# Performance work log

Hardware: AMD Instinct MI355X
Metric: run time of the kernel (lower is better)

## Reference

```python
import jax, jax.numpy as jnp
import numpy as np


def _chamfer(x, y):
    # x: [B, N, 3], y: [B, M, 3]
    x2 = jnp.sum(x * x, axis=-1)                      # [B, N]
    y2 = jnp.sum(y * y, axis=-1)                      # [B, M]
    xy = jnp.einsum('bnd,bmd->bnm', x, y)             # [B, N, M]
    d = x2[:, :, None] + y2[:, None, :] - 2.0 * xy    # [B, N, M]
    cham_x = jnp.min(d, axis=2).mean(axis=1)          # nearest y for each x
    cham_y = jnp.min(d, axis=1).mean(axis=1)          # nearest x for each y
    # pytorch3d default: mean over points, mean over batch, sum of both directions
    return jnp.mean(cham_x + cham_y)


def setup_inputs() -> dict:
    key = jax.random.key(0)
    kx, ky = jax.random.split(key)
    B, N, M, D = 4, 8192, 8192, 3
    x = jax.random.normal(kx, (B, N, D), dtype=jnp.float32)
    y = jax.random.normal(ky, (B, M, D), dtype=jnp.float32)
    return {"x": x, "y": y}


def reference(x, y):
    return _chamfer(x, y)
```

## Files before the change

### kernel.cpp

```cpp
#include <hip/hip_runtime.h>


#define BATCH   4
#define NPTS    8192
#define TPB     256
#define CSLICE  512
#define QT      4
#define QBLK    (4 * QT * 32)
#define MT      (CSLICE / 32)
#define SLICES  (NPTS / CSLICE)
#define QBLKS   (NPTS / QBLK)

typedef _Float16 h8   __attribute__((ext_vector_type(8)));
typedef float    f16v __attribute__((ext_vector_type(16)));

__device__ __forceinline__ void split16(float v, _Float16& hi, _Float16& lo) {
    hi = (_Float16)v;
    lo = (_Float16)(v - (float)hi);
}

__device__ __forceinline__ float tree16(const f16v& d) {
    float g0 = fminf(fminf(d[0],  d[1]),  d[2]);
    float g1 = fminf(fminf(d[3],  d[4]),  d[5]);
    float g2 = fminf(fminf(d[6],  d[7]),  d[8]);
    float g3 = fminf(fminf(d[9],  d[10]), d[11]);
    float g4 = fminf(fminf(d[12], d[13]), d[14]);
    float h0 = fminf(fminf(g0, g1), d[15]);
    float h1 = fminf(fminf(g2, g3), g4);
    return fminf(h0, h1);
}

__global__ __launch_bounds__(TPB, 8) void chamfer_mfma(const float* __restrict__ xg,
                                                       const float* __restrict__ yg,
                                                       float* __restrict__ partial,
                                                       float* __restrict__ out) {
    __shared__ h8 afrag[CSLICE * 2];

    const int tid    = threadIdx.x;
    const int qblock = blockIdx.x;
    const int slice  = blockIdx.y & (SLICES - 1);
    const int b      = blockIdx.y >> 4;
    const int dir    = blockIdx.z;
    const int lane   = tid & 63, wave = tid >> 6;
    const int col    = lane & 31, hv = lane >> 5;

    if (tid == 0) out[0] = 0.0f;
    const float* q = dir ? yg : xg;
    const float* r = dir ? xg : yg;

    const float* rbase = r + ((size_t)b * NPTS + slice * CSLICE) * 3;
#pragma unroll
    for (int i = 0; i < CSLICE / TPB; ++i) {
        const int p = tid + i * TPB;
        float r0 = rbase[p * 3 + 0], r1 = rbase[p * 3 + 1], r2 = rbase[p * 3 + 2];
        _Float16 h0, l0, h1, l1, h2, l2, rnh, rnl;
        split16(r0, h0, l0);
        split16(r1, h1, l1);
        split16(r2, h2, l2);
        split16(fmaf(r0, r0, fmaf(r1, r1, r2 * r2)), rnh, rnl);
        const int base = (p >> 5) * 64 + (p & 31);
        afrag[base]      = (h8){h0, h1, h2, l0, l1, l2, h0, h1};
        afrag[base + 32] = (h8){h2, rnh, rnl, (_Float16)1.0f, (_Float16)1.0f,
                                (_Float16)0.0f, (_Float16)0.0f, (_Float16)0.0f};
    }

    h8 bq[QT];
#pragma unroll
    for (int t = 0; t < QT; ++t) {
        const int qi = qblock * QBLK + (wave * QT + t) * 32 + col;
        const float* qp = q + ((size_t)b * NPTS + qi) * 3;
        float x0 = qp[0], x1 = qp[1], x2 = qp[2];
        _Float16 H0, L0, H1, L1, H2, L2, qnh, qnl;
        split16(-2.0f * x0, H0, L0);
        split16(-2.0f * x1, H1, L1);
        split16(-2.0f * x2, H2, L2);
        split16(fmaf(x0, x0, fmaf(x1, x1, x2 * x2)), qnh, qnl);
        h8 b0 = {H0, H1, H2, H0, H1, H2, L0, L1};
        h8 b1 = {L2, (_Float16)1.0f, (_Float16)1.0f, qnh, qnl,
                 (_Float16)0.0f, (_Float16)0.0f, (_Float16)0.0f};
        bq[t] = hv ? b1 : b0;
    }
    __syncthreads();

    float cm[QT];
#pragma unroll
    for (int t = 0; t < QT; ++t) cm[t] = 3.0e38f;

    for (int mt = 0; mt < MT; ++mt) {
        const h8 ar = afrag[mt * 64 + lane];
        f16v d0, d1;
        asm("v_mfma_f32_32x32x16_f16 %0, %2, %3, 0\n\t"
            "v_mfma_f32_32x32x16_f16 %1, %2, %4, 0\n\t"
            "s_nop 7\n\t"
            "s_nop 7"
            : "=v"(d0), "=v"(d1)
            : "v"(ar), "v"(bq[0]), "v"(bq[1]));
        cm[0] = fminf(cm[0], tree16(d0));
        cm[1] = fminf(cm[1], tree16(d1));

        f16v d2, d3;
        asm("v_mfma_f32_32x32x16_f16 %0, %2, %3, 0\n\t"
            "v_mfma_f32_32x32x16_f16 %1, %2, %4, 0\n\t"
            "s_nop 7\n\t"
            "s_nop 7"
            : "=v"(d2), "=v"(d3)
            : "v"(ar), "v"(bq[2]), "v"(bq[3]));
        cm[2] = fminf(cm[2], tree16(d2));
        cm[3] = fminf(cm[3], tree16(d3));
    }

    float* pp = partial + ((size_t)(dir * BATCH + b) * SLICES + slice) * NPTS
                        + qblock * QBLK;
#pragma unroll
    for (int t = 0; t < QT; ++t) {
        cm[t] = fminf(cm[t], __shfl_xor(cm[t], 32, 64));
        if (hv == 0)
            pp[(wave * QT + t) * 32 + col] = cm[t];
    }
}

__global__ __launch_bounds__(TPB) void chamfer_reduce(const float* __restrict__ partial,
                                                      float* __restrict__ out) {
    const int tid = threadIdx.x;
    const int g   = blockIdx.x * TPB + tid;
    const int db  = g >> 13;
    const int n   = g & (NPTS - 1);

    const float* p = partial + (size_t)db * SLICES * NPTS + n;
    float v = 3.0e38f;
#pragma unroll
    for (int s = 0; s < SLICES; ++s)
        v = fminf(v, p[(size_t)s * NPTS]);

    float w = v;
#pragma unroll
    for (int off = 32; off > 0; off >>= 1)
        w += __shfl_down(w, off, 64);
    __shared__ float ss[TPB / 64];
    if ((tid & 63) == 0) ss[tid >> 6] = w;
    __syncthreads();
    if (tid == 0)
        atomicAdd(out, (ss[0] + ss[1] + ss[2] + ss[3]) * (1.0f / (float)(BATCH * NPTS)));
}

extern "C" void kernel_launch(void* const* d_in, const int* in_sizes, int n_in,
                              void* d_out, int out_size, void* d_ws, size_t ws_size,
                              hipStream_t stream) {
    const float* x = (const float*)d_in[0];
    const float* y = (const float*)d_in[1];
    float* out = (float*)d_out;
    float* partial = (float*)d_ws;

    chamfer_mfma<<<dim3(QBLKS, BATCH * SLICES, 2), TPB, 0, stream>>>(x, y, partial, out);
    chamfer_reduce<<<dim3(2 * BATCH * NPTS / TPB), TPB, 0, stream>>>(partial, out);
}
```

Measured before the change: 77.36 us.

## Precompute fp16 split fragments once and fuse final reduction via last-block counter

Adds a presplit kernel that converts every point of x and y once into the hi/lo fp16 MFMA A and B fragments and stores them in workspace. The main kernel now copies those fragments straight into LDS and registers instead of recomputing the split per block. The separate reduce kernel is removed: each query-block group counts finished slices with an atomic counter, and the last block reduces the partial minima and adds into the output. This trades the redundant conversion and one launch for an extra launch, extra fragment traffic, and atomic/fence overhead.

```diff
diff --git a/kernel.cpp b/kernel.cpp
--- a/kernel.cpp
+++ b/kernel.cpp
@@ -10,6 +10,7 @@
 #define MT      (CSLICE / 32)
 #define SLICES  (NPTS / CSLICE)
 #define QBLKS   (NPTS / QBLK)
+#define FR_PER_SB 16384
 
 typedef _Float16 h8   __attribute__((ext_vector_type(8)));
 typedef float    f16v __attribute__((ext_vector_type(16)));
@@ -30,11 +31,53 @@
     return fminf(h0, h1);
 }
 
-__global__ __launch_bounds__(TPB, 8) void chamfer_mfma(const float* __restrict__ xg,
-                                                       const float* __restrict__ yg,
+__global__ __launch_bounds__(TPB) void chamfer_presplit(const float* __restrict__ xg,
+                                                        const float* __restrict__ yg,
+                                                        h8* __restrict__ aArr,
+                                                        h8* __restrict__ bArr,
+                                                        unsigned* __restrict__ cnt,
+                                                        float* __restrict__ out) {
+    const int tid = threadIdx.x;
+    const int g   = blockIdx.x * TPB + tid;
+    if (blockIdx.x == 0) {
+        if (tid < 2 * BATCH * QBLKS) cnt[tid] = 0u;
+        if (tid == 0) out[0] = 0.0f;
+    }
+    const int b = g >> 13, i = g & (NPTS - 1);
+#pragma unroll
+    for (int s = 0; s < 2; ++s) {
+        const float* p = (s ? yg : xg) + ((size_t)b * NPTS + i) * 3;
+        float c0 = p[0], c1 = p[1], c2 = p[2];
+        _Float16 h0, l0, h1, l1, h2, l2, nh, nl, H0, L0, H1, L1, H2, L2;
+        split16(c0, h0, l0);
+        split16(c1, h1, l1);
+        split16(c2, h2, l2);
+        split16(fmaf(c0, c0, fmaf(c1, c1, c2 * c2)), nh, nl);
+        split16(-2.0f * c0, H0, L0);
+        split16(-2.0f * c1, H1, L1);
+        split16(-2.0f * c2, H2, L2);
+        const size_t base = (size_t)(s * BATCH + b) * FR_PER_SB;
+        aArr[base + (i >> 5) * 64 + (i & 31)]      =
+            (h8){h0, h1, h2, l0, l1, l2, h0, h1};
+        aArr[base + (i >> 5) * 64 + 32 + (i & 31)] =
+            (h8){h2, nh, nl, (_Float16)1.0f, (_Float16)1.0f,
+                 (_Float16)0.0f, (_Float16)0.0f, (_Float16)0.0f};
+        bArr[base + i * 2]     =
+            (h8){H0, H1, H2, H0, H1, H2, L0, L1};
+        bArr[base + i * 2 + 1] =
+            (h8){L2, (_Float16)1.0f, (_Float16)1.0f, nh, nl,
+                 (_Float16)0.0f, (_Float16)0.0f, (_Float16)0.0f};
+    }
+}
+
+__global__ __launch_bounds__(TPB, 8) void chamfer_mfma(const h8* __restrict__ aArr,
+                                                       const h8* __restrict__ bArr,
                                                        float* __restrict__ partial,
+                                                       unsigned* __restrict__ cnt,
                                                        float* __restrict__ out) {
     __shared__ h8 afrag[CSLICE * 2];
+    __shared__ float sred[TPB / 64];
+    __shared__ int sflag;
 
     const int tid    = threadIdx.x;
     const int qblock = blockIdx.x;
@@ -44,41 +87,20 @@
     const int lane   = tid & 63, wave = tid >> 6;
     const int col    = lane & 31, hv = lane >> 5;
 
-    if (tid == 0) out[0] = 0.0f;
-    const float* q = dir ? yg : xg;
-    const float* r = dir ? xg : yg;
+    const int sa = dir ? 0 : 1;
+    const int sb = dir ? 1 : 0;
 
-    const float* rbase = r + ((size_t)b * NPTS + slice * CSLICE) * 3;
+    const h8* asrc = aArr + (size_t)(sa * BATCH + b) * FR_PER_SB + slice * (CSLICE * 2);
 #pragma unroll
-    for (int i = 0; i < CSLICE / TPB; ++i) {
-        const int p = tid + i * TPB;
-        float r0 = rbase[p * 3 + 0], r1 = rbase[p * 3 + 1], r2 = rbase[p * 3 + 2];
-        _Float16 h0, l0, h1, l1, h2, l2, rnh, rnl;
-        split16(r0, h0, l0);
-        split16(r1, h1, l1);
-        split16(r2, h2, l2);
-        split16(fmaf(r0, r0, fmaf(r1, r1, r2 * r2)), rnh, rnl);
-        const int base = (p >> 5) * 64 + (p & 31);
-        afrag[base]      = (h8){h0, h1, h2, l0, l1, l2, h0, h1};
-        afrag[base + 32] = (h8){h2, rnh, rnl, (_Float16)1.0f, (_Float16)1.0f,
-                                (_Float16)0.0f, (_Float16)0.0f, (_Float16)0.0f};
-    }
+    for (int i2 = 0; i2 < (CSLICE * 2) / TPB; ++i2)
+        afrag[tid + i2 * TPB] = asrc[tid + i2 * TPB];
 
+    const h8* bsrc = bArr + (size_t)(sb * BATCH + b) * FR_PER_SB;
     h8 bq[QT];
 #pragma unroll
     for (int t = 0; t < QT; ++t) {
         const int qi = qblock * QBLK + (wave * QT + t) * 32 + col;
-        const float* qp = q + ((size_t)b * NPTS + qi) * 3;
-        float x0 = qp[0], x1 = qp[1], x2 = qp[2];
-        _Float16 H0, L0, H1, L1, H2, L2, qnh, qnl;
-        split16(-2.0f * x0, H0, L0);
-        split16(-2.0f * x1, H1, L1);
-        split16(-2.0f * x2, H2, L2);
-        split16(fmaf(x0, x0, fmaf(x1, x1, x2 * x2)), qnh, qnl);
-        h8 b0 = {H0, H1, H2, H0, H1, H2, L0, L1};
-        h8 b1 = {L2, (_Float16)1.0f, (_Float16)1.0f, qnh, qnl,
-                 (_Float16)0.0f, (_Float16)0.0f, (_Float16)0.0f};
-        bq[t] = hv ? b1 : b0;
+        bq[t] = bsrc[qi * 2 + hv];
     }
     __syncthreads();
 
@@ -109,38 +131,46 @@
         cm[3] = fminf(cm[3], tree16(d3));
     }
 
-    float* pp = partial + ((size_t)(dir * BATCH + b) * SLICES + slice) * NPTS
+    float* pw = partial + ((size_t)(dir * BATCH + b) * SLICES + slice) * NPTS
                         + qblock * QBLK;
 #pragma unroll
     for (int t = 0; t < QT; ++t) {
         cm[t] = fminf(cm[t], __shfl_xor(cm[t], 32, 64));
         if (hv == 0)
-            pp[(wave * QT + t) * 32 + col] = cm[t];
+            pw[(wave * QT + t) * 32 + col] = cm[t];
     }
-}
 
-__global__ __launch_bounds__(TPB) void chamfer_reduce(const float* __restrict__ partial,
-                                                      float* __restrict__ out) {
-    const int tid = threadIdx.x;
-    const int g   = blockIdx.x * TPB + tid;
-    const int db  = g >> 13;
-    const int n   = g & (NPTS - 1);
+    __syncthreads();
+    const int group = (dir * BATCH + b) * QBLKS + qblock;
+    if (tid == 0) {
+        __threadfence();
+        unsigned old = __hip_atomic_fetch_add(&cnt[group], 1u, __ATOMIC_ACQ_REL,
+                                              __HIP_MEMORY_SCOPE_AGENT);
+        sflag = (old == (unsigned)(SLICES - 1)) ? 1 : 0;
+    }
+    __syncthreads();
+    if (!sflag) return;
 
-    const float* p = partial + (size_t)db * SLICES * NPTS + n;
-    float v = 3.0e38f;
+    const float* pr = partial + (size_t)(dir * BATCH + b) * SLICES * NPTS
+                              + qblock * QBLK;
+    float sum = 0.0f;
 #pragma unroll
-    for (int s = 0; s < SLICES; ++s)
-        v = fminf(v, p[(size_t)s * NPTS]);
-
-    float w = v;
+    for (int k = 0; k < QBLK / TPB; ++k) {
+        const int qq = tid + k * TPB;
+        float v = 3.0e38f;
+#pragma unroll
+        for (int sl = 0; sl < SLICES; ++sl)
+            v = fminf(v, pr[(size_t)sl * NPTS + qq]);
+        sum += v;
+    }
 #pragma unroll
     for (int off = 32; off > 0; off >>= 1)
-        w += __shfl_down(w, off, 64);
-    __shared__ float ss[TPB / 64];
-    if ((tid & 63) == 0) ss[tid >> 6] = w;
+        sum += __shfl_down(sum, off, 64);
+    if ((tid & 63) == 0) sred[tid >> 6] = sum;
     __syncthreads();
     if (tid == 0)
-        atomicAdd(out, (ss[0] + ss[1] + ss[2] + ss[3]) * (1.0f / (float)(BATCH * NPTS)));
+        atomicAdd(out, (sred[0] + sred[1] + sred[2] + sred[3])
+                           * (1.0f / (float)(BATCH * NPTS)));
 }
 
 extern "C" void kernel_launch(void* const* d_in, const int* in_sizes, int n_in,
@@ -149,8 +179,14 @@
     const float* x = (const float*)d_in[0];
     const float* y = (const float*)d_in[1];
     float* out = (float*)d_out;
-    float* partial = (float*)d_ws;
+    char* ws = (char*)d_ws;
+    float*    partial = (float*)ws;
+    h8*       aArr    = (h8*)(ws + (4u << 20));
+    h8*       bArr    = (h8*)(ws + (6u << 20));
+    unsigned* cnt     = (unsigned*)(ws + (8u << 20));
 
-    chamfer_mfma<<<dim3(QBLKS, BATCH * SLICES, 2), TPB, 0, stream>>>(x, y, partial, out);
-    chamfer_reduce<<<dim3(2 * BATCH * NPTS / TPB), TPB, 0, stream>>>(partial, out);
+    chamfer_presplit<<<dim3(BATCH * NPTS / TPB), TPB, 0, stream>>>(x, y, aArr, bArr,
+                                                                  cnt, out);
+    chamfer_mfma<<<dim3(QBLKS, BATCH * SLICES, 2), TPB, 0, stream>>>(aArr, bArr,
+                                                                    partial, cnt, out);
 }
```

Result: slower. 149.4 us (+93.1%).
